# Kernel optimization log

Hardware: AMD Instinct MI355X
Metric: run time of the kernel (lower is better)

## Reference

```python
import jax, jax.numpy as jnp
import numpy as np
import math

B, T, C = 8, 1024, 512
H = 8
HD = C // H  # 64
MAX_REL = 64 + 4  # args.block_size + args.time_cond


def setup_inputs() -> dict:
    key = jax.random.key(0)
    ks = jax.random.split(key, 12)
    xavier = lambda k, shape: jax.random.uniform(
        k, shape, jnp.float32, -1.0, 1.0) * math.sqrt(6.0 / (shape[0] + shape[1]))
    return {
        "x": jax.random.normal(ks[0], (B, T, C), jnp.float32),
        "Wq": xavier(ks[1], (C, C)), "bq": jnp.zeros((C,), jnp.float32),
        "Wk": xavier(ks[2], (C, C)), "bk": jnp.zeros((C,), jnp.float32),
        "Wv": xavier(ks[3], (C, C)), "bv": jnp.zeros((C,), jnp.float32),
        "Wo": xavier(ks[4], (C, C)), "bo": jnp.zeros((C,), jnp.float32),
        "rel_k": xavier(ks[5], (2 * MAX_REL + 1, HD)),
        "rel_v": xavier(ks[6], (2 * MAX_REL + 1, HD)),
    }


def _rel_index(t):
    # clipped relative distance matrix, shifted to [0, 2*MAX_REL]
    r = jnp.arange(t)
    dist = jnp.clip(r[None, :] - r[:, None], -MAX_REL, MAX_REL)
    return dist + MAX_REL  # (T, T) int32


def reference(x, Wq, bq, Wk, bk, Wv, bv, Wo, bo, rel_k, rel_v):
    b, t, c = x.shape
    h, hd = H, HD
    q = x @ Wq + bq
    k = x @ Wk + bk
    v = x @ Wv + bv
    rq = q.reshape(b, t, h, hd).transpose(0, 2, 1, 3)  # (B,H,T,hd)
    rk = k.reshape(b, t, h, hd).transpose(0, 2, 1, 3)
    rv = v.reshape(b, t, h, hd).transpose(0, 2, 1, 3)

    idx = _rel_index(t)                 # (T,T)
    rk2 = rel_k[idx]                    # (T,T,hd)
    rv2 = rel_v[idx]                    # (T,T,hd)

    attn1 = jnp.einsum("bhqd,bhkd->bhqk", rq, rk)
    attn2 = jnp.einsum("bhqd,qkd->bhqk", rq, rk2)
    # NOTE: original scales by 1/sqrt(embed_dim) (k.size(-1) == C), not head_dim
    attn = jax.nn.softmax((attn1 + attn2) * (1.0 / math.sqrt(c)), axis=-1)

    w1 = jnp.einsum("bhqk,bhkd->bhqd", attn, rv)
    w2 = jnp.einsum("bhqk,qkd->bhqd", attn, rv2)
    out = (w1 + w2).transpose(0, 2, 1, 3).reshape(b, t, c)
    return out @ Wo + bo
```

## Files before the change

### kernel.cpp

```cpp
#include <hip/hip_runtime.h>
#include <stdint.h>

#define Bb 8
#define Tt 1024
#define Cc 512
#define Hh 8
#define HD 64
#define MREL 68
#define NR 137
#define NRP 160
#define SCALE 0.044194173824159216f
#define KSCL  0.063763016845703125f

typedef unsigned short u16;
typedef unsigned int u32;
using u16x4  = __attribute__((ext_vector_type(4))) u16;
using u16x8  = __attribute__((ext_vector_type(8))) u16;
using u32x2  = __attribute__((ext_vector_type(2))) u32;
using f32x4  = __attribute__((ext_vector_type(4))) float;
using bf16x8 = __attribute__((ext_vector_type(8))) __bf16;

__device__ __forceinline__ u16 f2bf(float f) {
  u32 u = __builtin_bit_cast(u32, f);
  u += 0x7FFF + ((u >> 16) & 1);
  return (u16)(u >> 16);
}
__device__ __forceinline__ float bf2f(u16 v) {
  return __builtin_bit_cast(float, (u32)v << 16);
}
__device__ __forceinline__ bf16x8 as_bf8(u16x8 v) { return __builtin_bit_cast(bf16x8, v); }
__device__ __forceinline__ float fexp2(float x) {
  float r; asm("v_exp_f32 %0, %1" : "=v"(r) : "v"(x)); return r;
}
__device__ __forceinline__ u32 cvtpk(float lo, float hi) {
  u32 r; asm("v_cvt_pk_bf16_f32 %0, %1, %2" : "=v"(r) : "v"(lo), "v"(hi)); return r;
}

#define MFMA16(a, b, c) __builtin_amdgcn_mfma_f32_16x16x32_bf16((a), (b), (c), 0, 0, 0)

__global__ __launch_bounds__(256) void relv_prep(
    const float* __restrict__ rel_v, u16* __restrict__ rvT)
{
  int i = blockIdx.x * 256 + threadIdx.x;
  if (i < HD * NRP) {
    int d = i / NRP, r = i - d * NRP;
    rvT[i] = (r < NR) ? f2bf(rel_v[r * HD + d]) : (u16)0;
  }
}

__global__ __launch_bounds__(256) void w_prep(
    const float* __restrict__ Wq, const float* __restrict__ Wk,
    const float* __restrict__ Wv, const float* __restrict__ Wo,
    u16* __restrict__ WqT, u16* __restrict__ WkT,
    u16* __restrict__ WvT, u16* __restrict__ WoT)
{
  const float* W = blockIdx.y == 0 ? Wq : blockIdx.y == 1 ? Wk
                  : blockIdx.y == 2 ? Wv : Wo;
  u16* WT = blockIdx.y == 0 ? WqT : blockIdx.y == 1 ? WkT
           : blockIdx.y == 2 ? WvT : WoT;
  int i = blockIdx.x * 256 + threadIdx.x;
  int n = i >> 7, k4 = (i & 127) * 4;
  u16x4 o;
  #pragma unroll
  for (int j = 0; j < 4; ++j) o[j] = f2bf(W[(size_t)(k4 + j) * Cc + n]);
  *(u16x4*)&WT[(size_t)n * Cc + k4] = o;
}

__global__ __launch_bounds__(256) void qkv_gemm(
    const float* __restrict__ x,
    const u16* __restrict__ WqT, const u16* __restrict__ WkT,
    const u16* __restrict__ WvT,
    const float* __restrict__ bq, const float* __restrict__ bk,
    const float* __restrict__ bv,
    u16* __restrict__ Qb, u16* __restrict__ Kb, u16* __restrict__ VTb)
{
  __shared__ u16 Xs[64][40];
  __shared__ u16 WTs[3][64][40];

  const u16* Wp[3] = {WqT, WkT, WvT};
  const float* bp[3] = {bq, bk, bv};

  const int tid = threadIdx.x;
  const int wv_ = tid >> 6;
  const int l   = tid & 63;
  const int lr  = l & 15, lg = l >> 4;
  const int m0  = blockIdx.x * 64;
  const int n0  = blockIdx.y * 64;
  const int srow = tid >> 2, scol = (tid & 3) * 8;

  f32x4 acc[3][4];
  #pragma unroll
  for (int a = 0; a < 3; ++a)
    #pragma unroll
    for (int b = 0; b < 4; ++b) acc[a][b] = (f32x4){0.f, 0.f, 0.f, 0.f};

  for (int k0 = 0; k0 < Cc; k0 += 32) {
    {
      const float* xp = x + (size_t)(m0 + srow) * Cc + k0 + scol;
      f32x4 v0 = *(const f32x4*)xp;
      f32x4 v1 = *(const f32x4*)(xp + 4);
      u16x8 o = {f2bf(v0[0]), f2bf(v0[1]), f2bf(v0[2]), f2bf(v0[3]),
                 f2bf(v1[0]), f2bf(v1[1]), f2bf(v1[2]), f2bf(v1[3])};
      *(u16x8*)&Xs[srow][scol] = o;
    }
    #pragma unroll
    for (int q3 = 0; q3 < 3; ++q3) {
      u16x8 w = *(const u16x8*)(Wp[q3] + (size_t)(n0 + srow) * Cc + k0 + scol);
      *(u16x8*)&WTs[q3][srow][scol] = w;
    }
    __syncthreads();

    bf16x8 a = as_bf8(*(const u16x8*)&Xs[wv_ * 16 + lr][lg * 8]);
    #pragma unroll
    for (int q3 = 0; q3 < 3; ++q3) {
      #pragma unroll
      for (int nt = 0; nt < 4; ++nt) {
        bf16x8 b = as_bf8(*(const u16x8*)&WTs[q3][nt * 16 + lr][lg * 8]);
        acc[q3][nt] = MFMA16(a, b, acc[q3][nt]);
      }
    }
    __syncthreads();
  }

  const int bidx = m0 >> 10;
  #pragma unroll
  for (int q3 = 0; q3 < 3; ++q3) {
    #pragma unroll
    for (int nt = 0; nt < 4; ++nt) {
      int n = n0 + nt * 16 + lr;
      int h = n >> 6, d = n & 63;
      float bias = bp[q3][n];
      #pragma unroll
      for (int i = 0; i < 4; ++i) {
        int m = m0 + wv_ * 16 + lg * 4 + i;
        int t = m & (Tt - 1);
        u16 o = f2bf(acc[q3][nt][i] + bias);
        size_t bh = (size_t)(bidx * Hh + h);
        if (q3 == 0)      Qb[(bh * Tt + t) * HD + d] = o;
        else if (q3 == 1) Kb[(bh * Tt + t) * HD + d] = o;
        else              VTb[(bh * HD + d) * Tt + t] = o;
      }
    }
  }
}

__global__ __launch_bounds__(256, 6) void attn_kernel(
    const u16* __restrict__ Qb, const u16* __restrict__ Kb,
    const u16* __restrict__ VTb, const u16* __restrict__ rvT,
    const float* __restrict__ rel_k,
    u16* __restrict__ AO)
{
  __shared__ u16 P[16][264];
  __shared__ u16 S2[16][144];
  __shared__ u16 a2[16][168];
  __shared__ float red[3][4][16];
  __shared__ float rowrcp[16];

  const int tid = threadIdx.x;
  const int wv_ = tid >> 6, l = tid & 63;
  const int lr = l & 15, lg = l >> 4;
  const int bh = blockIdx.x;
  const int q0 = blockIdx.y * 16;
  const int bidx = bh >> 3, h = bh & 7;

  const u16* Qh = Qb  + (size_t)bh * Tt * HD;
  const u16* Kh = Kb  + (size_t)bh * Tt * HD;
  const u16* Vh = VTb + (size_t)bh * HD * Tt;

  bf16x8 aQ0 = as_bf8(*(const u16x8*)(Qh + (size_t)(q0 + lr) * HD + lg * 8));
  bf16x8 aQ1 = as_bf8(*(const u16x8*)(Qh + (size_t)(q0 + lr) * HD + 32 + lg * 8));

  const u16* kbase = Kh + (size_t)(wv_ * 16 + lr) * HD + lg * 8;
  u16x8 c0 = *(const u16x8*)(kbase);
  u16x8 c1 = *(const u16x8*)(kbase + 32);

  for (int i = tid; i < 16 * 168 / 2; i += 256) ((u32*)a2)[i] = 0;

  for (int ct = wv_; ct < 9; ct += 4) {
    int r = ct * 16 + lr;
    f32x4 acc = {0.f, 0.f, 0.f, 0.f};
    #pragma unroll
    for (int d0 = 0; d0 < 64; d0 += 32) {
      u16x8 bbits = {0, 0, 0, 0, 0, 0, 0, 0};
      if (r < NR) {
        f32x4 v0 = *(const f32x4*)(rel_k + (size_t)r * HD + d0 + lg * 8);
        f32x4 v1 = *(const f32x4*)(rel_k + (size_t)r * HD + d0 + lg * 8 + 4);
        bbits = (u16x8){f2bf(v0[0]), f2bf(v0[1]), f2bf(v0[2]), f2bf(v0[3]),
                        f2bf(v1[0]), f2bf(v1[1]), f2bf(v1[2]), f2bf(v1[3])};
      }
      acc = MFMA16(d0 ? aQ1 : aQ0, as_bf8(bbits), acc);
    }
    #pragma unroll
    for (int i = 0; i < 4; ++i)
      S2[lg * 4 + i][ct * 16 + lr] = f2bf(acc[i] * KSCL);
  }
  __syncthreads();

  const int qme = q0 + lr;
  const float cN = bf2f(S2[lr][0]);
  const float cP = bf2f(S2[lr][NR - 1]);

  int lowEnd  = (q0 >= 131) ? (((q0 - 131) >> 6) + 1) : 0;
  int hiStart = (q0 + 146) >> 6; if (hiStart > 16) hiStart = 16;

  float ps = 0.f, ps0 = 0.f, bnd = 0.f;
  const int kcb = wv_ * 16 + lg * 4;
  const u16* vrow = Vh + (size_t)(wv_ * 16 + lr) * Tt + lg * 8;

  f32x4 o0 = {0.f, 0.f, 0.f, 0.f}, o1 = {0.f, 0.f, 0.f, 0.f};

  for (int qtr = 0; qtr < 4; ++qtr) {
    #pragma unroll
    for (int t = 0; t < 4; ++t) {
      int kt = qtr * 4 + t;
      u16x8 n0{}, n1{};
      if (kt < 15) {
        n0 = *(const u16x8*)(kbase + (size_t)(kt + 1) * 64 * HD);
        n1 = *(const u16x8*)(kbase + (size_t)(kt + 1) * 64 * HD + 32);
      }
      f32x4 acc = {0.f, 0.f, 0.f, 0.f};
      acc = MFMA16(as_bf8(c0), aQ0, acc);
      acc = MFMA16(as_bf8(c1), aQ1, acc);
      int kc = kt * 64 + kcb;
      float p[4];
      if (kt >= lowEnd && kt < hiStart) {
        #pragma unroll
        for (int i = 0; i < 4; ++i) {
          int dr = kc + i - qme;
          int drc = dr < -MREL ? -MREL : (dr > MREL ? MREL : dr);
          float pe = fexp2(fmaf(acc[i], KSCL, bf2f(S2[lr][drc + MREL])));
          p[i] = pe;
          ps += pe;
          if (dr <= -MREL) ps0 += pe;
          if (dr >= -67 && dr <= 67) { a2[lr][dr + MREL] = f2bf(pe); bnd += pe; }
        }
      } else {
        float c = (kt < lowEnd) ? cN : cP;
        #pragma unroll
        for (int i = 0; i < 4; ++i) p[i] = fexp2(fmaf(acc[i], KSCL, c));
        float s4 = (p[0] + p[1]) + (p[2] + p[3]);
        ps += s4;
        if (kt < lowEnd) ps0 += s4;
      }
      u32x2 pw = {cvtpk(p[0], p[1]), cvtpk(p[2], p[3])};
      *(u32x2*)&P[lr][t * 64 + kcb] = pw;
      if (kt < 15) { c0 = n0; c1 = n1; }
    }
    __syncthreads();

    #pragma unroll
    for (int kp = 0; kp < 4; ++kp) {
      int kpg = qtr * 4 + kp;
      u16x8 vc0 = *(const u16x8*)(vrow + (size_t)kpg * 64);
      u16x8 vc1 = *(const u16x8*)(vrow + (size_t)kpg * 64 + 32);
      bf16x8 a0 = as_bf8(*(const u16x8*)&P[lr][kp * 64 + lg * 8]);
      bf16x8 a1 = as_bf8(*(const u16x8*)&P[lr][kp * 64 + 32 + lg * 8]);
      o0 = MFMA16(a0, as_bf8(vc0), o0);
      o1 = MFMA16(a1, as_bf8(vc1), o1);
    }
    __syncthreads();
  }

  ps  += __shfl_xor(ps, 16);  ps  += __shfl_xor(ps, 32);
  ps0 += __shfl_xor(ps0, 16); ps0 += __shfl_xor(ps0, 32);
  bnd += __shfl_xor(bnd, 16); bnd += __shfl_xor(bnd, 32);
  if (lg == 0) { red[0][wv_][lr] = ps; red[1][wv_][lr] = ps0; red[2][wv_][lr] = bnd; }
  __syncthreads();

  if (tid < 16) {
    float t0 = red[0][0][tid] + red[0][1][tid] + red[0][2][tid] + red[0][3][tid];
    float t1 = red[1][0][tid] + red[1][1][tid] + red[1][2][tid] + red[1][3][tid];
    float tb = red[2][0][tid] + red[2][1][tid] + red[2][2][tid] + red[2][3][tid];
    a2[tid][0]      = f2bf(t1);
    a2[tid][NR - 1] = f2bf(t0 - t1 - tb);
    rowrcp[tid] = 1.0f / t0;
  }
  __syncthreads();

  #pragma unroll
  for (int j = 0; j < 5; ++j) {
    u16x8 brv = *(const u16x8*)(rvT + (size_t)(wv_ * 16 + lr) * NRP + j * 32 + lg * 8);
    bf16x8 aa = as_bf8(*(const u16x8*)&a2[lr][j * 32 + lg * 8]);
    if (j & 1) o1 = MFMA16(aa, as_bf8(brv), o1);
    else       o0 = MFMA16(aa, as_bf8(brv), o0);
  }

  #pragma unroll
  for (int i = 0; i < 4; ++i) {
    int row = lg * 4 + i;
    float val = (o0[i] + o1[i]) * rowrcp[row];
    int t = q0 + row, cc = h * HD + wv_ * 16 + lr;
    AO[((size_t)(bidx * Tt + t)) * Cc + cc] = f2bf(val);
  }
}

__global__ __launch_bounds__(256) void out_gemm(
    const u16* __restrict__ AO, const u16* __restrict__ WoT,
    const float* __restrict__ bo, float* __restrict__ out)
{
  __shared__ u16 As[64][40];
  __shared__ u16 WTs[64][40];
  const int tid = threadIdx.x;
  const int wv_ = tid >> 6, l = tid & 63, lr = l & 15, lg = l >> 4;
  const int m0 = blockIdx.x * 64, n0 = blockIdx.y * 64;
  const int srow = tid >> 2, scol = (tid & 3) * 8;

  f32x4 acc[4];
  #pragma unroll
  for (int b = 0; b < 4; ++b) acc[b] = (f32x4){0.f, 0.f, 0.f, 0.f};

  for (int k0 = 0; k0 < Cc; k0 += 32) {
    u16x8 av = *(const u16x8*)(AO + (size_t)(m0 + srow) * Cc + k0 + scol);
    *(u16x8*)&As[srow][scol] = av;
    u16x8 wv2 = *(const u16x8*)(WoT + (size_t)(n0 + srow) * Cc + k0 + scol);
    *(u16x8*)&WTs[srow][scol] = wv2;
    __syncthreads();

    bf16x8 a = as_bf8(*(const u16x8*)&As[wv_ * 16 + lr][lg * 8]);
    #pragma unroll
    for (int nt = 0; nt < 4; ++nt) {
      bf16x8 b = as_bf8(*(const u16x8*)&WTs[nt * 16 + lr][lg * 8]);
      acc[nt] = MFMA16(a, b, acc[nt]);
    }
    __syncthreads();
  }

  #pragma unroll
  for (int nt = 0; nt < 4; ++nt) {
    int n = n0 + nt * 16 + lr;
    float bias = bo[n];
    #pragma unroll
    for (int i = 0; i < 4; ++i) {
      int m = m0 + wv_ * 16 + lg * 4 + i;
      out[(size_t)m * Cc + n] = acc[nt][i] + bias;
    }
  }
}

extern "C" void kernel_launch(void* const* d_in, const int* in_sizes, int n_in,
                              void* d_out, int out_size, void* d_ws, size_t ws_size,
                              hipStream_t stream) {
  const float* x  = (const float*)d_in[0];
  const float* Wq = (const float*)d_in[1];
  const float* bq = (const float*)d_in[2];
  const float* Wk = (const float*)d_in[3];
  const float* bk = (const float*)d_in[4];
  const float* Wv = (const float*)d_in[5];
  const float* bv = (const float*)d_in[6];
  const float* Wo = (const float*)d_in[7];
  const float* bo = (const float*)d_in[8];
  const float* rk = (const float*)d_in[9];
  const float* rv = (const float*)d_in[10];

  const size_t BHTD = (size_t)Bb * Hh * Tt * HD;
  const size_t WSZ  = (size_t)Cc * Cc;

  u16* Qb = (u16*)d_out;
  u16* Kb = Qb + BHTD;
  u16* VT  = (u16*)d_ws;
  u16* AO  = VT + BHTD;
  u16* rvT = AO + BHTD;
  u16* WqT = rvT + (size_t)HD * NRP;
  u16* WkT = WqT + WSZ;
  u16* WvT = WkT + WSZ;
  u16* WoT = WvT + WSZ;
  float* outf = (float*)d_out;

  relv_prep<<<dim3((HD * NRP + 255) / 256), 256, 0, stream>>>(rv, rvT);
  w_prep<<<dim3(256, 4), 256, 0, stream>>>(Wq, Wk, Wv, Wo, WqT, WkT, WvT, WoT);
  qkv_gemm<<<dim3(128, 8), 256, 0, stream>>>(x, WqT, WkT, WvT, bq, bk, bv, Qb, Kb, VT);
  attn_kernel<<<dim3(64, 64), 256, 0, stream>>>(Qb, Kb, VT, rvT, rk, AO);
  out_gemm<<<dim3(128, 8), 256, 0, stream>>>(AO, WoT, bo, outf);
}
```

Baseline: 209.8 us.

## Restructure attention to 32-row query tiles with 32x32 MFMA and split-K waves

The attention kernel now processes 32 query rows per block with 32x32x16 MFMAs. Each wave owns a quarter of the key range and keeps P in registers, feeding the PV MFMA directly instead of staging it through shared memory. Per-wave partial outputs are merged with LDS atomics before normalization. This removes the per-quarter block barriers and the P round-trip through LDS and halves the grid. The cost is lower occupancy (launch bound 3), float atomics in LDS, and strided 4-element V loads.

```diff
diff --git a/kernel.cpp b/kernel.cpp
--- a/kernel.cpp
+++ b/kernel.cpp
@@ -16,8 +16,9 @@
 typedef unsigned int u32;
 using u16x4  = __attribute__((ext_vector_type(4))) u16;
 using u16x8  = __attribute__((ext_vector_type(8))) u16;
-using u32x2  = __attribute__((ext_vector_type(2))) u32;
+using u32x4  = __attribute__((ext_vector_type(4))) u32;
 using f32x4  = __attribute__((ext_vector_type(4))) float;
+using f32x16 = __attribute__((ext_vector_type(16))) float;
 using bf16x8 = __attribute__((ext_vector_type(8))) __bf16;
 
 __device__ __forceinline__ u16 f2bf(float f) {
@@ -29,14 +30,25 @@
   return __builtin_bit_cast(float, (u32)v << 16);
 }
 __device__ __forceinline__ bf16x8 as_bf8(u16x8 v) { return __builtin_bit_cast(bf16x8, v); }
+__device__ __forceinline__ bf16x8 frag4(u32 w0, u32 w1, u32 w2, u32 w3) {
+  u32x4 v = {w0, w1, w2, w3};
+  return __builtin_bit_cast(bf16x8, v);
+}
 __device__ __forceinline__ float fexp2(float x) {
   float r; asm("v_exp_f32 %0, %1" : "=v"(r) : "v"(x)); return r;
 }
 __device__ __forceinline__ u32 cvtpk(float lo, float hi) {
   u32 r; asm("v_cvt_pk_bf16_f32 %0, %1, %2" : "=v"(r) : "v"(lo), "v"(hi)); return r;
 }
+__device__ __forceinline__ bf16x8 ldsplit(const u16* base) {
+  u16x4 lo = *(const u16x4*)(base);
+  u16x4 hi = *(const u16x4*)(base + 8);
+  u16x8 r = {lo[0], lo[1], lo[2], lo[3], hi[0], hi[1], hi[2], hi[3]};
+  return as_bf8(r);
+}
 
 #define MFMA16(a, b, c) __builtin_amdgcn_mfma_f32_16x16x32_bf16((a), (b), (c), 0, 0, 0)
+#define MFMA32(a, b, c) __builtin_amdgcn_mfma_f32_32x32x16_bf16((a), (b), (c), 0, 0, 0)
 
 __global__ __launch_bounds__(256) void relv_prep(
     const float* __restrict__ rel_v, u16* __restrict__ rvT)
@@ -144,153 +156,164 @@
   }
 }
 
-__global__ __launch_bounds__(256, 6) void attn_kernel(
+__global__ __launch_bounds__(256, 3) void attn_kernel(
     const u16* __restrict__ Qb, const u16* __restrict__ Kb,
     const u16* __restrict__ VTb, const u16* __restrict__ rvT,
     const float* __restrict__ rel_k,
     u16* __restrict__ AO)
 {
-  __shared__ u16 P[16][264];
-  __shared__ u16 S2[16][144];
-  __shared__ u16 a2[16][168];
-  __shared__ float red[3][4][16];
-  __shared__ float rowrcp[16];
+  __shared__ u16 S2L[32][144];
+  __shared__ u16 a2L[32][176];
+  __shared__ float Obuf[32][64];
+  __shared__ float red[3][4][32];
+  __shared__ float rowrcp[32];
 
   const int tid = threadIdx.x;
   const int wv_ = tid >> 6, l = tid & 63;
-  const int lr = l & 15, lg = l >> 4;
+  const int l31 = l & 31, hi = l >> 5;
+  const int lr16 = l & 15, lg16 = l >> 4;
   const int bh = blockIdx.x;
-  const int q0 = blockIdx.y * 16;
+  const int q0 = blockIdx.y * 32;
   const int bidx = bh >> 3, h = bh & 7;
 
   const u16* Qh = Qb  + (size_t)bh * Tt * HD;
   const u16* Kh = Kb  + (size_t)bh * Tt * HD;
   const u16* Vh = VTb + (size_t)bh * HD * Tt;
 
-  bf16x8 aQ0 = as_bf8(*(const u16x8*)(Qh + (size_t)(q0 + lr) * HD + lg * 8));
-  bf16x8 aQ1 = as_bf8(*(const u16x8*)(Qh + (size_t)(q0 + lr) * HD + 32 + lg * 8));
-
-  const u16* kbase = Kh + (size_t)(wv_ * 16 + lr) * HD + lg * 8;
-  u16x8 c0 = *(const u16x8*)(kbase);
-  u16x8 c1 = *(const u16x8*)(kbase + 32);
-
-  for (int i = tid; i < 16 * 168 / 2; i += 256) ((u32*)a2)[i] = 0;
-
-  for (int ct = wv_; ct < 9; ct += 4) {
-    int r = ct * 16 + lr;
-    f32x4 acc = {0.f, 0.f, 0.f, 0.f};
-    #pragma unroll
-    for (int d0 = 0; d0 < 64; d0 += 32) {
-      u16x8 bbits = {0, 0, 0, 0, 0, 0, 0, 0};
-      if (r < NR) {
-        f32x4 v0 = *(const f32x4*)(rel_k + (size_t)r * HD + d0 + lg * 8);
-        f32x4 v1 = *(const f32x4*)(rel_k + (size_t)r * HD + d0 + lg * 8 + 4);
-        bbits = (u16x8){f2bf(v0[0]), f2bf(v0[1]), f2bf(v0[2]), f2bf(v0[3]),
-                        f2bf(v1[0]), f2bf(v1[1]), f2bf(v1[2]), f2bf(v1[3])};
+  for (int i = tid; i < 32 * 176 / 2; i += 256) ((u32*)a2L)[i] = 0;
+  for (int i = tid; i < 32 * 64; i += 256) ((float*)Obuf)[i] = 0.f;
+
+  #pragma unroll
+  for (int h16 = 0; h16 < 2; ++h16) {
+    bf16x8 aQ0 = as_bf8(*(const u16x8*)(Qh + (size_t)(q0 + h16 * 16 + lr16) * HD + lg16 * 8));
+    bf16x8 aQ1 = as_bf8(*(const u16x8*)(Qh + (size_t)(q0 + h16 * 16 + lr16) * HD + 32 + lg16 * 8));
+    for (int ct = wv_; ct < 9; ct += 4) {
+      int r = ct * 16 + lr16;
+      f32x4 acc = {0.f, 0.f, 0.f, 0.f};
+      #pragma unroll
+      for (int d0 = 0; d0 < 64; d0 += 32) {
+        u16x8 bbits = {0, 0, 0, 0, 0, 0, 0, 0};
+        if (r < NR) {
+          f32x4 v0 = *(const f32x4*)(rel_k + (size_t)r * HD + d0 + lg16 * 8);
+          f32x4 v1 = *(const f32x4*)(rel_k + (size_t)r * HD + d0 + lg16 * 8 + 4);
+          bbits = (u16x8){f2bf(v0[0]), f2bf(v0[1]), f2bf(v0[2]), f2bf(v0[3]),
+                          f2bf(v1[0]), f2bf(v1[1]), f2bf(v1[2]), f2bf(v1[3])};
+        }
+        acc = MFMA16(d0 ? aQ1 : aQ0, as_bf8(bbits), acc);
       }
-      acc = MFMA16(d0 ? aQ1 : aQ0, as_bf8(bbits), acc);
-    }
-    #pragma unroll
-    for (int i = 0; i < 4; ++i)
-      S2[lg * 4 + i][ct * 16 + lr] = f2bf(acc[i] * KSCL);
+      #pragma unroll
+      for (int i = 0; i < 4; ++i)
+        S2L[h16 * 16 + lg16 * 4 + i][ct * 16 + lr16] = f2bf(acc[i] * KSCL);
+    }
   }
   __syncthreads();
 
-  const int qme = q0 + lr;
-  const float cN = bf2f(S2[lr][0]);
-  const float cP = bf2f(S2[lr][NR - 1]);
-
-  int lowEnd  = (q0 >= 131) ? (((q0 - 131) >> 6) + 1) : 0;
-  int hiStart = (q0 + 146) >> 6; if (hiStart > 16) hiStart = 16;
-
+  const int qme = q0 + l31;
+  const float cN = bf2f(S2L[l31][0]);
+  const float cP = bf2f(S2L[l31][NR - 1]);
+
+  bf16x8 qf[4];
+  #pragma unroll
+  for (int s = 0; s < 4; ++s)
+    qf[s] = as_bf8(*(const u16x8*)(Qh + (size_t)qme * HD + 16 * s + 8 * hi));
+
+  const int wk0 = wv_ * 256;
+  f32x16 oA = {}, oB = {};
   float ps = 0.f, ps0 = 0.f, bnd = 0.f;
-  const int kcb = wv_ * 16 + lg * 4;
-  const u16* vrow = Vh + (size_t)(wv_ * 16 + lr) * Tt + lg * 8;
-
-  f32x4 o0 = {0.f, 0.f, 0.f, 0.f}, o1 = {0.f, 0.f, 0.f, 0.f};
-
-  for (int qtr = 0; qtr < 4; ++qtr) {
-    #pragma unroll
-    for (int t = 0; t < 4; ++t) {
-      int kt = qtr * 4 + t;
-      u16x8 n0{}, n1{};
-      if (kt < 15) {
-        n0 = *(const u16x8*)(kbase + (size_t)(kt + 1) * 64 * HD);
-        n1 = *(const u16x8*)(kbase + (size_t)(kt + 1) * 64 * HD + 32);
+
+  #pragma unroll
+  for (int t = 0; t < 8; ++t) {
+    const int kc0 = wk0 + 32 * t;
+    bf16x8 kf[4];
+    #pragma unroll
+    for (int s = 0; s < 4; ++s)
+      kf[s] = as_bf8(*(const u16x8*)(Kh + (size_t)(kc0 + l31) * HD + 16 * s + 8 * hi));
+
+    f32x16 acc = {};
+    #pragma unroll
+    for (int s = 0; s < 4; ++s) acc = MFMA32(kf[s], qf[s], acc);
+
+    float p[16];
+    const bool isLow  = (kc0 <= q0 - 99);
+    const bool isHigh = (kc0 >= q0 + 99);
+    if (isLow | isHigh) {
+      const float c = isLow ? cN : cP;
+      #pragma unroll
+      for (int r = 0; r < 16; ++r) p[r] = fexp2(fmaf(acc[r], KSCL, c));
+      float s16 = ((p[0]+p[1])+(p[2]+p[3])) + ((p[4]+p[5])+(p[6]+p[7]))
+                + ((p[8]+p[9])+(p[10]+p[11])) + ((p[12]+p[13])+(p[14]+p[15]));
+      ps += s16;
+      if (isLow) ps0 += s16;
+    } else {
+      #pragma unroll
+      for (int r = 0; r < 16; ++r) {
+        int kcoff = (r & 3) + 8 * (r >> 2) + 4 * hi;
+        int dr = kc0 + kcoff - qme;
+        int drc = dr < -MREL ? -MREL : (dr > MREL ? MREL : dr);
+        float pe = fexp2(fmaf(acc[r], KSCL, bf2f(S2L[l31][drc + MREL])));
+        p[r] = pe;
+        ps += pe;
+        if (dr <= -MREL) ps0 += pe;
+        if (dr >= -67 && dr <= 67) { a2L[l31][dr + MREL] = f2bf(pe); bnd += pe; }
       }
-      f32x4 acc = {0.f, 0.f, 0.f, 0.f};
-      acc = MFMA16(as_bf8(c0), aQ0, acc);
-      acc = MFMA16(as_bf8(c1), aQ1, acc);
-      int kc = kt * 64 + kcb;
-      float p[4];
-      if (kt >= lowEnd && kt < hiStart) {
-        #pragma unroll
-        for (int i = 0; i < 4; ++i) {
-          int dr = kc + i - qme;
-          int drc = dr < -MREL ? -MREL : (dr > MREL ? MREL : dr);
-          float pe = fexp2(fmaf(acc[i], KSCL, bf2f(S2[lr][drc + MREL])));
-          p[i] = pe;
-          ps += pe;
-          if (dr <= -MREL) ps0 += pe;
-          if (dr >= -67 && dr <= 67) { a2[lr][dr + MREL] = f2bf(pe); bnd += pe; }
-        }
-      } else {
-        float c = (kt < lowEnd) ? cN : cP;
-        #pragma unroll
-        for (int i = 0; i < 4; ++i) p[i] = fexp2(fmaf(acc[i], KSCL, c));
-        float s4 = (p[0] + p[1]) + (p[2] + p[3]);
-        ps += s4;
-        if (kt < lowEnd) ps0 += s4;
-      }
-      u32x2 pw = {cvtpk(p[0], p[1]), cvtpk(p[2], p[3])};
-      *(u32x2*)&P[lr][t * 64 + kcb] = pw;
-      if (kt < 15) { c0 = n0; c1 = n1; }
-    }
-    __syncthreads();
-
-    #pragma unroll
-    for (int kp = 0; kp < 4; ++kp) {
-      int kpg = qtr * 4 + kp;
-      u16x8 vc0 = *(const u16x8*)(vrow + (size_t)kpg * 64);
-      u16x8 vc1 = *(const u16x8*)(vrow + (size_t)kpg * 64 + 32);
-      bf16x8 a0 = as_bf8(*(const u16x8*)&P[lr][kp * 64 + lg * 8]);
-      bf16x8 a1 = as_bf8(*(const u16x8*)&P[lr][kp * 64 + 32 + lg * 8]);
-      o0 = MFMA16(a0, as_bf8(vc0), o0);
-      o1 = MFMA16(a1, as_bf8(vc1), o1);
-    }
-    __syncthreads();
-  }
-
-  ps  += __shfl_xor(ps, 16);  ps  += __shfl_xor(ps, 32);
-  ps0 += __shfl_xor(ps0, 16); ps0 += __shfl_xor(ps0, 32);
-  bnd += __shfl_xor(bnd, 16); bnd += __shfl_xor(bnd, 32);
-  if (lg == 0) { red[0][wv_][lr] = ps; red[1][wv_][lr] = ps0; red[2][wv_][lr] = bnd; }
+    }
+
+    bf16x8 paLo = frag4(cvtpk(p[0], p[1]),  cvtpk(p[2], p[3]),
+                        cvtpk(p[4], p[5]),  cvtpk(p[6], p[7]));
+    bf16x8 paHi = frag4(cvtpk(p[8], p[9]),  cvtpk(p[10], p[11]),
+                        cvtpk(p[12], p[13]), cvtpk(p[14], p[15]));
+
+    const u16* vA = Vh + (size_t)l31 * Tt;
+    const u16* vB = Vh + (size_t)(32 + l31) * Tt;
+    bf16x8 vA0 = ldsplit(vA + kc0 + 4 * hi);
+    bf16x8 vA1 = ldsplit(vA + kc0 + 16 + 4 * hi);
+    bf16x8 vB0 = ldsplit(vB + kc0 + 4 * hi);
+    bf16x8 vB1 = ldsplit(vB + kc0 + 16 + 4 * hi);
+    oA = MFMA32(paLo, vA0, oA);
+    oA = MFMA32(paHi, vA1, oA);
+    oB = MFMA32(paLo, vB0, oB);
+    oB = MFMA32(paHi, vB1, oB);
+  }
+
+  ps  += __shfl_xor(ps, 32);
+  ps0 += __shfl_xor(ps0, 32);
+  bnd += __shfl_xor(bnd, 32);
+  if (l < 32) { red[0][wv_][l] = ps; red[1][wv_][l] = ps0; red[2][wv_][l] = bnd; }
   __syncthreads();
 
-  if (tid < 16) {
+  if (tid < 32) {
     float t0 = red[0][0][tid] + red[0][1][tid] + red[0][2][tid] + red[0][3][tid];
     float t1 = red[1][0][tid] + red[1][1][tid] + red[1][2][tid] + red[1][3][tid];
     float tb = red[2][0][tid] + red[2][1][tid] + red[2][2][tid] + red[2][3][tid];
-    a2[tid][0]      = f2bf(t1);
-    a2[tid][NR - 1] = f2bf(t0 - t1 - tb);
+    a2L[tid][0]      = f2bf(t1);
+    a2L[tid][NR - 1] = f2bf(t0 - t1 - tb);
     rowrcp[tid] = 1.0f / t0;
   }
   __syncthreads();
 
-  #pragma unroll
-  for (int j = 0; j < 5; ++j) {
-    u16x8 brv = *(const u16x8*)(rvT + (size_t)(wv_ * 16 + lr) * NRP + j * 32 + lg * 8);
-    bf16x8 aa = as_bf8(*(const u16x8*)&a2[lr][j * 32 + lg * 8]);
-    if (j & 1) o1 = MFMA16(aa, as_bf8(brv), o1);
-    else       o0 = MFMA16(aa, as_bf8(brv), o0);
-  }
-
-  #pragma unroll
-  for (int i = 0; i < 4; ++i) {
-    int row = lg * 4 + i;
-    float val = (o0[i] + o1[i]) * rowrcp[row];
-    int t = q0 + row, cc = h * HD + wv_ * 16 + lr;
-    AO[((size_t)(bidx * Tt + t)) * Cc + cc] = f2bf(val);
+  for (int W = wv_; W < 10; W += 4) {
+    bf16x8 aa = as_bf8(*(const u16x8*)&a2L[l31][W * 16 + 8 * hi]);
+    bf16x8 rA = as_bf8(*(const u16x8*)(rvT + (size_t)l31 * NRP        + W * 16 + 8 * hi));
+    bf16x8 rB = as_bf8(*(const u16x8*)(rvT + (size_t)(32 + l31) * NRP + W * 16 + 8 * hi));
+    oA = MFMA32(aa, rA, oA);
+    oB = MFMA32(aa, rB, oB);
+  }
+
+  #pragma unroll
+  for (int r = 0; r < 16; ++r) {
+    int qoff = (r & 3) + 8 * (r >> 2) + 4 * hi;
+    atomicAdd(&Obuf[qoff][l31], oA[r]);
+    atomicAdd(&Obuf[qoff][32 + l31], oB[r]);
+  }
+  __syncthreads();
+
+  {
+    int rq = tid >> 3, d8 = (tid & 7) * 8;
+    float rc = rowrcp[rq];
+    u16x8 o;
+    #pragma unroll
+    for (int j = 0; j < 8; ++j) o[j] = f2bf(Obuf[rq][d8 + j] * rc);
+    *(u16x8*)&AO[((size_t)(bidx * Tt + q0 + rq)) * Cc + h * HD + d8] = o;
   }
 }
 
@@ -369,6 +392,6 @@
   relv_prep<<<dim3((HD * NRP + 255) / 256), 256, 0, stream>>>(rv, rvT);
   w_prep<<<dim3(256, 4), 256, 0, stream>>>(Wq, Wk, Wv, Wo, WqT, WkT, WvT, WoT);
   qkv_gemm<<<dim3(128, 8), 256, 0, stream>>>(x, WqT, WkT, WvT, bq, bk, bv, Qb, Kb, VT);
-  attn_kernel<<<dim3(64, 64), 256, 0, stream>>>(Qb, Kb, VT, rvT, rk, AO);
+  attn_kernel<<<dim3(64, 32), 256, 0, stream>>>(Qb, Kb, VT, rvT, rk, AO);
   out_gemm<<<dim3(128, 8), 256, 0, stream>>>(AO, WoT, bo, outf);
 }
```

Result: slower. 249.5 us (+18.9%).
